# Performance work log

Measured on AMD Instinct MI355X. Metric: run time of the kernel, lower is better.

The kernel has to match this reference:

```python
import jax, jax.numpy as jnp
import numpy as np

N, H, E, T = 100000, 128, 500000, 6  # nodes, hidden, max edges, edge types


def setup_inputs() -> dict:
    key = jax.random.key(0)
    ks = jax.random.split(key, 16)
    xav_e = float(np.sqrt(6.0 / (H + T * H)))  # xavier_uniform for edge_dense
    xav_h = float(np.sqrt(6.0 / (H + H)))
    u = lambda k, s, a: jax.random.uniform(k, s, jnp.float32, -a, a)
    return {
        "node_embeddings": jax.random.normal(ks[0], (N, H), jnp.float32),
        "W_edge": u(ks[1], (H, T * H), xav_e),
        "b_edge": 1e-6 * jax.random.normal(ks[2], (T * H,), jnp.float32),
        "W_ir": u(ks[3], (H, H), xav_h), "b_ir": jnp.zeros((H,), jnp.float32),
        "W_iz": u(ks[4], (H, H), xav_h), "b_iz": jnp.zeros((H,), jnp.float32),
        "W_in": u(ks[5], (H, H), xav_h), "b_in": jnp.zeros((H,), jnp.float32),
        "W_hr": u(ks[6], (H, H), xav_h),
        "W_hz": u(ks[7], (H, H), xav_h),
        "W_hn": u(ks[8], (H, H), xav_h), "b_hn": jnp.zeros((H,), jnp.float32),
        "source_indices": jax.random.randint(ks[9], (E,), 0, N, jnp.int32),
        "dest_indices": jax.random.randint(ks[10], (E,), 0, N, jnp.int32),
        "edge_types": jax.random.randint(ks[11], (E,), 0, T, jnp.int32),
        "num_edges": 450000,
    }


def reference(node_embeddings, W_edge, b_edge, W_ir, b_ir, W_iz, b_iz,
              W_in, b_in, W_hr, W_hz, W_hn, b_hn,
              source_indices, dest_indices, edge_types, num_edges):
    num_nodes, hidden = node_embeddings.shape
    max_edges = edge_types.shape[0]
    # gather source nodes, project to all edge types at once: [E, T*H]
    src = node_embeddings[source_indices]
    all_types = (src @ W_edge + b_edge).reshape(max_edges, -1, hidden)  # [E,T,H]
    # select per-edge type
    msg = jnp.take_along_axis(all_types, edge_types[:, None, None], axis=1)[:, 0, :]
    # mask padding edges, scatter-add into destination nodes
    msg = jnp.where((jnp.arange(max_edges) < num_edges)[:, None], msg, 0)
    agg = jax.ops.segment_sum(msg, dest_indices, num_segments=num_nodes)
    # GRU update: carry h = aggregated messages, inputs x = node_embeddings
    h, x = agg, node_embeddings
    r = jax.nn.sigmoid(x @ W_ir + b_ir + h @ W_hr)
    z = jax.nn.sigmoid(x @ W_iz + b_iz + h @ W_hz)
    n = jnp.tanh(x @ W_in + b_in + r * (h @ W_hn + b_hn))
    return (1.0 - z) * n + z * h
```

## Files before the change

### kernel.cpp

```cpp
#include <hip/hip_runtime.h>
#include <hip/hip_bf16.h>

#define HD 128
#define NT 6

typedef unsigned short u16;
typedef unsigned int u32;
typedef __attribute__((ext_vector_type(8))) short bf16x8;
typedef __attribute__((ext_vector_type(4))) float f32x4;

__device__ __forceinline__ float sigmoidf_(float x) {
  return 1.0f / (1.0f + __expf(-x));
}

__device__ __forceinline__ u16 f2bf(float x) {
  u32 u = __float_as_uint(x);
  return (u16)((u + 0x7FFFu + ((u >> 16) & 1u)) >> 16);
}
__device__ __forceinline__ float bflo(u32 v) { return __uint_as_float(v << 16); }
__device__ __forceinline__ float bfhi(u32 v) { return __uint_as_float(v & 0xffff0000u); }

__device__ __forceinline__ int swz(int p) { return p ^ (((p >> 8) & 7) << 4); }

__global__ void k_cvt_w(const float* __restrict__ We,
                        const float* __restrict__ Wir, const float* __restrict__ Wiz,
                        const float* __restrict__ Win, const float* __restrict__ Whr,
                        const float* __restrict__ Whz, const float* __restrict__ Whn,
                        u16* __restrict__ WeT, u16* __restrict__ WgT) {
  int i = blockIdx.x * blockDim.x + threadIdx.x;
  if (i < NT * HD * HD) {
    int c = i >> 7, k = i & 127;
    WeT[i] = f2bf(We[(size_t)k * (NT * HD) + c]);
  } else {
    int j = i - NT * HD * HD;
    if (j < 6 * HD * HD) {
      int m = j >> 14, jj = j & 16383;
      int c = jj >> 7, k = jj & 127;
      const float* W = (m == 0) ? Wir : (m == 1) ? Wiz : (m == 2) ? Win
                     : (m == 3) ? Whr : (m == 4) ? Whz : Whn;
      WgT[j] = f2bf(W[(size_t)k * HD + c]);
    }
  }
}

__global__ __launch_bounds__(256) void k_gemm_edge6(
    const float* __restrict__ X, const u16* __restrict__ WeT,
    const float* __restrict__ Be, u16* __restrict__ P, int N)
{
  __shared__ char As[32768];
  __shared__ char Bs[32768];
  const int tid = threadIdx.x;
  const int row0 = blockIdx.x * 128;

  #pragma unroll
  for (int i = 0; i < 8; ++i) {
    int p = i * 4096 + tid * 16;
    int row = row0 + (p >> 8);
    union { u16 u[8]; bf16x8 v; } ra;
    if (row < N) {
      const float4* s = (const float4*)(X + (size_t)row0 * HD + (p >> 1));
      float4 f0 = s[0], f1 = s[1];
      ra.u[0] = f2bf(f0.x); ra.u[1] = f2bf(f0.y); ra.u[2] = f2bf(f0.z); ra.u[3] = f2bf(f0.w);
      ra.u[4] = f2bf(f1.x); ra.u[5] = f2bf(f1.y); ra.u[6] = f2bf(f1.z); ra.u[7] = f2bf(f1.w);
    } else {
      #pragma unroll
      for (int j = 0; j < 8; ++j) ra.u[j] = 0;
    }
    *(bf16x8*)(As + swz(p)) = ra.v;
  }

  const int l = tid & 63, w = tid >> 6;
  const int m0 = (w >> 1) * 64, n0 = (w & 1) * 64;
  const int lr = l & 15, lg = l >> 4;
  f32x4 zero = {0.f, 0.f, 0.f, 0.f};

  for (int t = 0; t < NT; ++t) {
    __syncthreads();
    const char* gB = (const char*)(WeT + (size_t)t * HD * HD);
    #pragma unroll
    for (int i = 0; i < 8; ++i) {
      int p = i * 4096 + tid * 16;
      *(bf16x8*)(Bs + swz(p)) = *(const bf16x8*)(gB + p);
    }
    __syncthreads();

    f32x4 acc[4][4];
    #pragma unroll
    for (int m = 0; m < 4; ++m)
      #pragma unroll
      for (int n = 0; n < 4; ++n) acc[m][n] = zero;

    #pragma unroll
    for (int k = 0; k < 4; ++k) {
      bf16x8 a[4], b[4];
      #pragma unroll
      for (int m = 0; m < 4; ++m)
        a[m] = *(const bf16x8*)(As + swz((m0 + m * 16 + lr) * 256 + k * 64 + lg * 16));
      #pragma unroll
      for (int n = 0; n < 4; ++n)
        b[n] = *(const bf16x8*)(Bs + swz((n0 + n * 16 + lr) * 256 + k * 64 + lg * 16));
      #pragma unroll
      for (int m = 0; m < 4; ++m)
        #pragma unroll
        for (int n = 0; n < 4; ++n)
          acc[m][n] = __builtin_amdgcn_mfma_f32_16x16x32_bf16(a[m], b[n], acc[m][n], 0, 0, 0);
    }

    float bias[4];
    #pragma unroll
    for (int n = 0; n < 4; ++n) bias[n] = Be[t * HD + n0 + n * 16 + lr];
    #pragma unroll
    for (int m = 0; m < 4; ++m) {
      int rbase = row0 + m0 + m * 16 + lg * 4;
      #pragma unroll
      for (int j = 0; j < 4; ++j) {
        int row = rbase + j;
        if (row < N) {
          #pragma unroll
          for (int n = 0; n < 4; ++n)
            P[(size_t)row * (NT * HD) + t * HD + n0 + n * 16 + lr] =
                f2bf(acc[m][n][j] + bias[n]);
        }
      }
    }
  }
}

__global__ __launch_bounds__(256) void k_count(const int* __restrict__ dst,
                                               const int* __restrict__ nePtr,
                                               int* __restrict__ deg) {
  const int ne = nePtr[0];
  for (int e = blockIdx.x * blockDim.x + threadIdx.x; e < ne;
       e += gridDim.x * blockDim.x)
    atomicAdd(&deg[dst[e]], 1);
}

__global__ __launch_bounds__(256) void k_scan_a(const int* __restrict__ deg,
                                                int* __restrict__ off,
                                                int* __restrict__ bsum, int N) {
  __shared__ int s[256];
  const int b = blockIdx.x, tid = threadIdx.x;
  const int base = b * 1024 + tid * 4;
  int v0 = 0, v1 = 0, v2 = 0, v3 = 0;
  if (base < N) v0 = deg[base];
  if (base + 1 < N) v1 = deg[base + 1];
  if (base + 2 < N) v2 = deg[base + 2];
  if (base + 3 < N) v3 = deg[base + 3];
  const int sum = v0 + v1 + v2 + v3;
  s[tid] = sum;
  __syncthreads();
  for (int d = 1; d < 256; d <<= 1) {
    int t = (tid >= d) ? s[tid - d] : 0;
    __syncthreads();
    s[tid] += t;
    __syncthreads();
  }
  const int excl = s[tid] - sum;
  if (base < N) off[base] = excl;
  if (base + 1 < N) off[base + 1] = excl + v0;
  if (base + 2 < N) off[base + 2] = excl + v0 + v1;
  if (base + 3 < N) off[base + 3] = excl + v0 + v1 + v2;
  if (tid == 255) bsum[b] = s[255];
}

__global__ void k_scan_b(int* __restrict__ bsum, int nb) {
  __shared__ int s[1024];
  const int tid = threadIdx.x;
  const int v = (tid < nb) ? bsum[tid] : 0;
  s[tid] = v;
  __syncthreads();
  for (int d = 1; d < 1024; d <<= 1) {
    int t = (tid >= d) ? s[tid - d] : 0;
    __syncthreads();
    s[tid] += t;
    __syncthreads();
  }
  if (tid < nb) bsum[tid] = s[tid] - v;
}

__global__ __launch_bounds__(256) void k_scan_c(int* __restrict__ off,
                                                const int* __restrict__ bsum, int N) {
  const int b = blockIdx.x, tid = threadIdx.x;
  const int add = bsum[b];
  const int base = b * 1024 + tid * 4;
  #pragma unroll
  for (int i = 0; i < 4; ++i)
    if (base + i < N) off[base + i] += add;
}

__global__ __launch_bounds__(256) void k_fill(const int* __restrict__ src,
                                              const int* __restrict__ dst,
                                              const int* __restrict__ typ,
                                              const int* __restrict__ nePtr,
                                              int* __restrict__ off,
                                              u32* __restrict__ elist) {
  const int ne = nePtr[0];
  for (int e = blockIdx.x * blockDim.x + threadIdx.x; e < ne;
       e += gridDim.x * blockDim.x) {
    int pos = atomicAdd(&off[dst[e]], 1);
    elist[pos] = (u32)(src[e] * NT + typ[e]);
  }
}

__global__ __launch_bounds__(256) void k_gather(
    const u16* __restrict__ P, const int* __restrict__ deg,
    const int* __restrict__ off, const u32* __restrict__ elist,
    u16* __restrict__ Hb, int N)
{
  const int l = threadIdx.x & 63;
  int wid = (int)((blockIdx.x * blockDim.x + threadIdx.x) >> 6);
  int nw = (int)((gridDim.x * blockDim.x) >> 6);
  for (int n = wid; n < N; n += nw) {
    const int e1 = off[n];
    const int e0 = e1 - deg[n];
    float a0 = 0.f, a1 = 0.f, b0 = 0.f, b1 = 0.f;
    for (int e = e0; e < e1; e += 4) {
      u32 p0 = elist[e];
      u32 p1 = (e + 1 < e1) ? elist[e + 1] : p0;
      u32 p2 = (e + 2 < e1) ? elist[e + 2] : p0;
      u32 p3 = (e + 3 < e1) ? elist[e + 3] : p0;
      u32 v0 = *((const u32*)(P + (size_t)p0 * HD) + l);
      u32 v1 = *((const u32*)(P + (size_t)p1 * HD) + l);
      u32 v2 = *((const u32*)(P + (size_t)p2 * HD) + l);
      u32 v3 = *((const u32*)(P + (size_t)p3 * HD) + l);
      if (e + 1 >= e1) v1 = 0;
      if (e + 2 >= e1) v2 = 0;
      if (e + 3 >= e1) v3 = 0;
      a0 += bflo(v0); a1 += bfhi(v0);
      b0 += bflo(v1); b1 += bfhi(v1);
      a0 += bflo(v2); a1 += bfhi(v2);
      b0 += bflo(v3); b1 += bfhi(v3);
    }
    a0 += b0; a1 += b1;
    u32 hp = ((u32)f2bf(a1) << 16) | (u32)f2bf(a0);
    *((u32*)(Hb + (size_t)n * HD) + l) = hp;
  }
}

__global__ __launch_bounds__(512, 2) void k_gru3(
    const float* __restrict__ X, const u16* __restrict__ Hb,
    const u16* __restrict__ WgT,
    const float* __restrict__ bir, const float* __restrict__ biz,
    const float* __restrict__ bin_, const float* __restrict__ bhn,
    float* __restrict__ out, int N)
{
  __shared__ char Xs[32768];
  __shared__ char Hs[32768];
  __shared__ char Wb[2][32768];
  const int tid = threadIdx.x;
  const int row0 = blockIdx.x * 128;
  const int l = tid & 63, w = tid >> 6;
  const int lr = l & 15, lg = l >> 4;
  const int rloc = w * 16;

  #pragma unroll
  for (int i = 0; i < 4; ++i) {
    int p = i * 8192 + tid * 16;
    int row = row0 + (p >> 8);
    union { u16 u[8]; bf16x8 v; } rx, rh;
    if (row < N) {
      const float4* sx = (const float4*)(X + (size_t)row0 * HD + (p >> 1));
      float4 x0 = sx[0], x1 = sx[1];
      rx.u[0] = f2bf(x0.x); rx.u[1] = f2bf(x0.y); rx.u[2] = f2bf(x0.z); rx.u[3] = f2bf(x0.w);
      rx.u[4] = f2bf(x1.x); rx.u[5] = f2bf(x1.y); rx.u[6] = f2bf(x1.z); rx.u[7] = f2bf(x1.w);
      rh.v = *(const bf16x8*)((const char*)Hb + (size_t)row0 * 256 + p);
    } else {
      #pragma unroll
      for (int j = 0; j < 8; ++j) { rx.u[j] = 0; rh.u[j] = 0; }
    }
    *(bf16x8*)(Xs + swz(p)) = rx.v;
    *(bf16x8*)(Hs + swz(p)) = rh.v;
  }

  bf16x8 wreg[4];
  auto loadW = [&](int g) {
    const char* gp = (const char*)(WgT + (size_t)g * HD * HD);
    #pragma unroll
    for (int i = 0; i < 4; ++i)
      wreg[i] = *(const bf16x8*)(gp + i * 8192 + tid * 16);
  };
  auto writeW = [&](int buf) {
    #pragma unroll
    for (int i = 0; i < 4; ++i) {
      int p = i * 8192 + tid * 16;
      *(bf16x8*)(Wb[buf] + swz(p)) = wreg[i];
    }
  };

  f32x4 zero = {0.f, 0.f, 0.f, 0.f};
  auto sweepL = [&](const char* Ab, const char* Wp, f32x4* acc) {
    #pragma unroll
    for (int n = 0; n < 8; ++n) acc[n] = zero;
    #pragma unroll
    for (int k = 0; k < 4; ++k) {
      bf16x8 a = *(const bf16x8*)(Ab + swz((rloc + lr) * 256 + k * 64 + lg * 16));
      #pragma unroll
      for (int n = 0; n < 8; ++n) {
        bf16x8 b = *(const bf16x8*)(Wp + swz((n * 16 + lr) * 256 + k * 64 + lg * 16));
        acc[n] = __builtin_amdgcn_mfma_f32_16x16x32_bf16(a, b, acc[n], 0, 0, 0);
      }
    }
  };

  f32x4 t1[8], t2[8], rg[8], nn[8];
  float bv[8];

  loadW(0); writeW(0);
  __syncthreads();

  loadW(3);
  sweepL(Xs, Wb[0], t1);
  writeW(1);
  __syncthreads();

  loadW(5);
  sweepL(Hs, Wb[1], t2);
  writeW(0);
  #pragma unroll
  for (int n = 0; n < 8; ++n) bv[n] = bir[n * 16 + lr];
  #pragma unroll
  for (int n = 0; n < 8; ++n)
    #pragma unroll
    for (int j = 0; j < 4; ++j) rg[n][j] = sigmoidf_(t1[n][j] + bv[n] + t2[n][j]);
  __syncthreads();

  loadW(2);
  sweepL(Hs, Wb[0], t2);
  writeW(1);
  #pragma unroll
  for (int n = 0; n < 8; ++n) bv[n] = bhn[n * 16 + lr];
  #pragma unroll
  for (int n = 0; n < 8; ++n)
    #pragma unroll
    for (int j = 0; j < 4; ++j) rg[n][j] *= (t2[n][j] + bv[n]);
  __syncthreads();

  loadW(1);
  sweepL(Xs, Wb[1], t1);
  writeW(0);
  #pragma unroll
  for (int n = 0; n < 8; ++n) bv[n] = bin_[n * 16 + lr];
  #pragma unroll
  for (int n = 0; n < 8; ++n)
    #pragma unroll
    for (int j = 0; j < 4; ++j) nn[n][j] = tanhf(t1[n][j] + bv[n] + rg[n][j]);
  __syncthreads();

  loadW(4);
  sweepL(Xs, Wb[0], t1);
  writeW(1);
  __syncthreads();

  sweepL(Hs, Wb[1], t2);
  #pragma unroll
  for (int n = 0; n < 8; ++n) bv[n] = biz[n * 16 + lr];
  #pragma unroll
  for (int n = 0; n < 8; ++n) {
    #pragma unroll
    for (int j = 0; j < 4; ++j) {
      int row = row0 + rloc + lg * 4 + j;
      if (row < N) {
        int col = n * 16 + lr;
        float z = sigmoidf_(t1[n][j] + bv[n] + t2[n][j]);
        u16 hu = Hb[(size_t)row * HD + col];
        float h = __uint_as_float((u32)hu << 16);
        out[(size_t)row * HD + col] = (1.0f - z) * nn[n][j] + z * h;
      }
    }
  }
}

__global__ __launch_bounds__(256) void k_gather_gru(
    const float* __restrict__ X, const u16* __restrict__ P,
    const int* __restrict__ deg, const int* __restrict__ off,
    const u32* __restrict__ elist, const u16* __restrict__ WgT,
    const float* __restrict__ bir, const float* __restrict__ biz,
    const float* __restrict__ bin_, const float* __restrict__ bhn,
    float* __restrict__ out, int N)
{
  __shared__ char Xs[16384];
  __shared__ char Hs[16384];
  const int tid = threadIdx.x;
  const int l = tid & 63, w = tid >> 6;
  const int row0 = blockIdx.x * 64;
  const int wr0 = w * 16;

  #pragma unroll
  for (int it = 0; it < 4; ++it) {
    int chunk = it * 64 + l;
    int r = chunk >> 4, seg = chunk & 15;
    int grow = row0 + wr0 + r;
    union { u16 u[8]; bf16x8 v; } rx;
    if (grow < N) {
      const float4* sx = (const float4*)(X + (size_t)grow * HD + seg * 8);
      float4 x0 = sx[0], x1 = sx[1];
      rx.u[0] = f2bf(x0.x); rx.u[1] = f2bf(x0.y); rx.u[2] = f2bf(x0.z); rx.u[3] = f2bf(x0.w);
      rx.u[4] = f2bf(x1.x); rx.u[5] = f2bf(x1.y); rx.u[6] = f2bf(x1.z); rx.u[7] = f2bf(x1.w);
    } else {
      #pragma unroll
      for (int j = 0; j < 8; ++j) rx.u[j] = 0;
    }
    *(bf16x8*)(Xs + swz((wr0 + r) * 256 + seg * 16)) = rx.v;
  }

  for (int i = 0; i < 16; ++i) {
    int n = row0 + wr0 + i;
    float a0 = 0.f, a1 = 0.f;
    if (n < N) {
      int e1 = off[n];
      for (int e = e1 - deg[n]; e < e1; e += 4) {
        u32 p0 = elist[e];
        u32 p1 = (e + 1 < e1) ? elist[e + 1] : p0;
        u32 p2 = (e + 2 < e1) ? elist[e + 2] : p0;
        u32 p3 = (e + 3 < e1) ? elist[e + 3] : p0;
        u32 v0 = *((const u32*)(P + (size_t)p0 * HD) + l);
        u32 v1 = *((const u32*)(P + (size_t)p1 * HD) + l);
        u32 v2 = *((const u32*)(P + (size_t)p2 * HD) + l);
        u32 v3 = *((const u32*)(P + (size_t)p3 * HD) + l);
        if (e + 1 >= e1) v1 = 0;
        if (e + 2 >= e1) v2 = 0;
        if (e + 3 >= e1) v3 = 0;
        a0 += bflo(v0) + bflo(v1) + bflo(v2) + bflo(v3);
        a1 += bfhi(v0) + bfhi(v1) + bfhi(v2) + bfhi(v3);
      }
    }
    u32 hp = ((u32)f2bf(a1) << 16) | (u32)f2bf(a0);
    *(u32*)(Hs + swz((wr0 + i) * 256 + l * 4)) = hp;
  }

  const int lr = l & 15, lg = l >> 4;
  const int rloc = wr0;

  f32x4 zero = {0.f, 0.f, 0.f, 0.f};
  auto sweep = [&](const char* Ab, const u16* WT, f32x4* acc) {
    #pragma unroll
    for (int n = 0; n < 8; ++n) acc[n] = zero;
    #pragma unroll
    for (int k = 0; k < 4; ++k) {
      bf16x8 a = *(const bf16x8*)(Ab + swz((rloc + lr) * 256 + k * 64 + lg * 16));
      #pragma unroll
      for (int n = 0; n < 8; ++n) {
        bf16x8 b = *(const bf16x8*)(WT + (size_t)(n * 16 + lr) * HD + k * 32 + lg * 8);
        acc[n] = __builtin_amdgcn_mfma_f32_16x16x32_bf16(a, b, acc[n], 0, 0, 0);
      }
    }
  };

  f32x4 t1[8], t2[8], rg[8], nn[8];
  float bv[8];

  sweep(Xs, WgT + 0 * HD * HD, t1);
  sweep(Hs, WgT + 3 * HD * HD, t2);
  #pragma unroll
  for (int n = 0; n < 8; ++n) bv[n] = bir[n * 16 + lr];
  #pragma unroll
  for (int n = 0; n < 8; ++n)
    #pragma unroll
    for (int j = 0; j < 4; ++j) rg[n][j] = sigmoidf_(t1[n][j] + bv[n] + t2[n][j]);

  sweep(Hs, WgT + 5 * HD * HD, t2);
  #pragma unroll
  for (int n = 0; n < 8; ++n) bv[n] = bhn[n * 16 + lr];
  #pragma unroll
  for (int n = 0; n < 8; ++n)
    #pragma unroll
    for (int j = 0; j < 4; ++j) rg[n][j] *= (t2[n][j] + bv[n]);

  sweep(Xs, WgT + 2 * HD * HD, t1);
  #pragma unroll
  for (int n = 0; n < 8; ++n) bv[n] = bin_[n * 16 + lr];
  #pragma unroll
  for (int n = 0; n < 8; ++n)
    #pragma unroll
    for (int j = 0; j < 4; ++j) nn[n][j] = tanhf(t1[n][j] + bv[n] + rg[n][j]);

  sweep(Xs, WgT + 1 * HD * HD, t1);
  sweep(Hs, WgT + 4 * HD * HD, t2);
  #pragma unroll
  for (int n = 0; n < 8; ++n) bv[n] = biz[n * 16 + lr];
  #pragma unroll
  for (int n = 0; n < 8; ++n) {
    #pragma unroll
    for (int j = 0; j < 4; ++j) {
      int row = row0 + rloc + lg * 4 + j;
      if (row < N) {
        float z = sigmoidf_(t1[n][j] + bv[n] + t2[n][j]);
        u16 hu = *(const u16*)(Hs + swz((rloc + lg * 4 + j) * 256 + (n * 16 + lr) * 2));
        float h = __uint_as_float((u32)hu << 16);
        out[(size_t)row * HD + n * 16 + lr] = (1.0f - z) * nn[n][j] + z * h;
      }
    }
  }
}

__global__ __launch_bounds__(256) void k_scatter(
    const u16* __restrict__ P, const int* __restrict__ src,
    const int* __restrict__ dst, const int* __restrict__ typ,
    const int* __restrict__ nePtr, float* __restrict__ agg,
    int ldP, int fixedType)
{
  const int ne = nePtr[0];
  const int lane = threadIdx.x & 63;
  const int wid = (int)((blockIdx.x * blockDim.x + threadIdx.x) >> 6);
  const int nw = (int)((gridDim.x * blockDim.x) >> 6);
  for (int e = wid; e < ne; e += nw) {
    const int t = typ[e];
    if (fixedType >= 0 && t != fixedType) continue;
    const size_t po = (ldP == HD) ? (size_t)src[e] * HD
                                  : (size_t)src[e] * (NT * HD) + (size_t)t * HD;
    u32 v = *(const u32*)(P + po + lane * 2);
    float* o = agg + (size_t)dst[e] * HD + lane * 2;
    unsafeAtomicAdd(o, bflo(v));
    unsafeAtomicAdd(o + 1, bfhi(v));
  }
}

__global__ __launch_bounds__(256) void k_gru(
    const float* __restrict__ X, const float* __restrict__ agg,
    const u16* __restrict__ WgT,
    const float* __restrict__ bir, const float* __restrict__ biz,
    const float* __restrict__ bin_, const float* __restrict__ bhn,
    float* __restrict__ out, int N)
{
  __shared__ char Xs[16384];
  __shared__ char Hs[16384];
  const int tid = threadIdx.x;
  const int row0 = blockIdx.x * 64;

  #pragma unroll
  for (int i = 0; i < 4; ++i) {
    int p = i * 4096 + tid * 16;
    int row = row0 + (p >> 8);
    union { u16 u[8]; bf16x8 v; } rx, rh;
    if (row < N) {
      const float4* sx = (const float4*)(X + (size_t)row0 * HD + (p >> 1));
      const float4* sh = (const float4*)(agg + (size_t)row0 * HD + (p >> 1));
      float4 x0 = sx[0], x1 = sx[1], h0 = sh[0], h1 = sh[1];
      rx.u[0] = f2bf(x0.x); rx.u[1] = f2bf(x0.y); rx.u[2] = f2bf(x0.z); rx.u[3] = f2bf(x0.w);
      rx.u[4] = f2bf(x1.x); rx.u[5] = f2bf(x1.y); rx.u[6] = f2bf(x1.z); rx.u[7] = f2bf(x1.w);
      rh.u[0] = f2bf(h0.x); rh.u[1] = f2bf(h0.y); rh.u[2] = f2bf(h0.z); rh.u[3] = f2bf(h0.w);
      rh.u[4] = f2bf(h1.x); rh.u[5] = f2bf(h1.y); rh.u[6] = f2bf(h1.z); rh.u[7] = f2bf(h1.w);
    } else {
      #pragma unroll
      for (int j = 0; j < 8; ++j) { rx.u[j] = 0; rh.u[j] = 0; }
    }
    *(bf16x8*)(Xs + swz(p)) = rx.v;
    *(bf16x8*)(Hs + swz(p)) = rh.v;
  }
  __syncthreads();

  const int l = tid & 63, w = tid >> 6;
  const int lr = l & 15, lg = l >> 4;
  const int rloc = w * 16;

  f32x4 zero = {0.f, 0.f, 0.f, 0.f};
  auto sweep = [&](const char* Ab, const u16* WT, f32x4* acc) {
    #pragma unroll
    for (int n = 0; n < 8; ++n) acc[n] = zero;
    #pragma unroll
    for (int k = 0; k < 4; ++k) {
      bf16x8 a = *(const bf16x8*)(Ab + swz((rloc + lr) * 256 + k * 64 + lg * 16));
      #pragma unroll
      for (int n = 0; n < 8; ++n) {
        bf16x8 b = *(const bf16x8*)(WT + (size_t)(n * 16 + lr) * HD + k * 32 + lg * 8);
        acc[n] = __builtin_amdgcn_mfma_f32_16x16x32_bf16(a, b, acc[n], 0, 0, 0);
      }
    }
  };

  f32x4 t1[8], t2[8], rg[8], nn[8];
  float bv[8];

  sweep(Xs, WgT + 0 * HD * HD, t1);
  sweep(Hs, WgT + 3 * HD * HD, t2);
  #pragma unroll
  for (int n = 0; n < 8; ++n) bv[n] = bir[n * 16 + lr];
  #pragma unroll
  for (int n = 0; n < 8; ++n)
    #pragma unroll
    for (int j = 0; j < 4; ++j) rg[n][j] = sigmoidf_(t1[n][j] + bv[n] + t2[n][j]);

  sweep(Hs, WgT + 5 * HD * HD, t2);
  #pragma unroll
  for (int n = 0; n < 8; ++n) bv[n] = bhn[n * 16 + lr];
  #pragma unroll
  for (int n = 0; n < 8; ++n)
    #pragma unroll
    for (int j = 0; j < 4; ++j) rg[n][j] *= (t2[n][j] + bv[n]);

  sweep(Xs, WgT + 2 * HD * HD, t1);
  #pragma unroll
  for (int n = 0; n < 8; ++n) bv[n] = bin_[n * 16 + lr];
  #pragma unroll
  for (int n = 0; n < 8; ++n)
    #pragma unroll
    for (int j = 0; j < 4; ++j) nn[n][j] = tanhf(t1[n][j] + bv[n] + rg[n][j]);

  sweep(Xs, WgT + 1 * HD * HD, t1);
  sweep(Hs, WgT + 4 * HD * HD, t2);
  #pragma unroll
  for (int n = 0; n < 8; ++n) bv[n] = biz[n * 16 + lr];
  #pragma unroll
  for (int n = 0; n < 8; ++n) {
    #pragma unroll
    for (int j = 0; j < 4; ++j) {
      int row = row0 + rloc + lg * 4 + j;
      if (row < N) {
        float z = sigmoidf_(t1[n][j] + bv[n] + t2[n][j]);
        float h = agg[(size_t)row * HD + n * 16 + lr];
        out[(size_t)row * HD + n * 16 + lr] = (1.0f - z) * nn[n][j] + z * h;
      }
    }
  }
}

extern "C" void kernel_launch(void* const* d_in, const int* in_sizes, int n_in,
                              void* d_out, int out_size, void* d_ws, size_t ws_size,
                              hipStream_t stream) {
  const float* X      = (const float*)d_in[0];
  const float* W_edge = (const float*)d_in[1];
  const float* b_edge = (const float*)d_in[2];
  const float* b_ir   = (const float*)d_in[4];
  const float* b_iz   = (const float*)d_in[6];
  const float* b_in   = (const float*)d_in[8];
  const float* b_hn   = (const float*)d_in[12];
  const int* src      = (const int*)d_in[13];
  const int* dst      = (const int*)d_in[14];
  const int* typ      = (const int*)d_in[15];
  const int* nePtr    = (const int*)d_in[16];

  const int N = in_sizes[0] / HD;
  const int E = in_sizes[13];
  char* ws = (char*)d_ws;

  size_t cur = 0;
  auto alloc = [&](size_t bytes) {
    size_t p = cur;
    cur = (cur + bytes + 255) & ~(size_t)255;
    return p;
  };
  u16* WeT   = (u16*)(ws + alloc((size_t)NT * HD * HD * 2));
  u16* WgT   = (u16*)(ws + alloc((size_t)6 * HD * HD * 2));
  int* deg   = (int*)(ws + alloc((size_t)N * 4));
  int* offA  = (int*)(ws + alloc((size_t)N * 4));
  int* bsum  = (int*)(ws + alloc(1024 * 4));
  u32* elist = (u32*)(ws + alloc((size_t)E * 4));
  size_t base_need = cur;
  u16* P     = (u16*)(ws + alloc((size_t)N * NT * HD * 2));
  const size_t csr_need = cur;
  u16* Hb    = (u16*)(ws + alloc((size_t)N * HD * 2));
  const size_t split_need = cur;

  const int gb = (N + 127) / 128;
  const int NB = (N + 1023) / 1024;

  k_cvt_w<<<(NT * HD * HD + 6 * HD * HD + 255) / 256, 256, 0, stream>>>(
      W_edge, (const float*)d_in[3], (const float*)d_in[5], (const float*)d_in[7],
      (const float*)d_in[9], (const float*)d_in[10], (const float*)d_in[11], WeT, WgT);

  if (ws_size >= csr_need) {
    hipMemsetAsync(deg, 0, (size_t)N * 4, stream);
    k_gemm_edge6<<<gb, 256, 0, stream>>>(X, WeT, b_edge, P, N);
    k_count<<<1024, 256, 0, stream>>>(dst, nePtr, deg);
    k_scan_a<<<NB, 256, 0, stream>>>(deg, offA, bsum, N);
    k_scan_b<<<1, 1024, 0, stream>>>(bsum, NB);
    k_scan_c<<<NB, 256, 0, stream>>>(offA, bsum, N);
    k_fill<<<1024, 256, 0, stream>>>(src, dst, typ, nePtr, offA, elist);
    if (ws_size >= split_need) {
      k_gather<<<(N + 3) / 4, 256, 0, stream>>>(P, deg, offA, elist, Hb, N);
      k_gru3<<<gb, 512, 0, stream>>>(
          X, Hb, WgT, b_ir, b_iz, b_in, b_hn, (float*)d_out, N);
    } else {
      k_gather_gru<<<(N + 63) / 64, 256, 0, stream>>>(
          X, P, deg, offA, elist, WgT, b_ir, b_iz, b_in, b_hn, (float*)d_out, N);
    }
  } else {
    float* agg = (float*)d_out;
    hipMemsetAsync(d_out, 0, (size_t)out_size * sizeof(float), stream);
    size_t pneed = base_need + (size_t)N * NT * HD * 2;
    if (ws_size >= pneed) {
      u16* Pf = (u16*)(ws + base_need);
      k_gemm_edge6<<<gb, 256, 0, stream>>>(X, WeT, b_edge, Pf, N);
      k_scatter<<<2048, 256, 0, stream>>>(Pf, src, dst, typ, nePtr, agg, NT * HD, -1);
      k_gru<<<(N + 63) / 64, 256, 0, stream>>>(X, agg, WgT, b_ir, b_iz, b_in, b_hn, agg, N);
    }
  }
}
```

Measured before the change: 253.6 us.

## Retile GRU kernel to 2x4 MFMA warp tiles with single-buffered weights

The GRU kernel now assigns each of the 8 waves a 32x64 output tile (2x4 MFMA blocks) instead of a 16x128 strip, so each wave's A and B fragment loads are reused across more MFMAs and fewer LDS reads are issued per MFMA. The double-buffered register-prefetched weight pipeline is replaced by one shared weight buffer staged with syncs before and after each load, which frees 32KB of LDS and drops the occupancy hint in launch bounds. The cost is that weight loads no longer overlap with compute, which adds sync stalls per gate matrix.

```diff
diff --git a/kernel.cpp b/kernel.cpp
--- a/kernel.cpp
+++ b/kernel.cpp
@@ -19,6 +19,7 @@
 }
 __device__ __forceinline__ float bflo(u32 v) { return __uint_as_float(v << 16); }
 __device__ __forceinline__ float bfhi(u32 v) { return __uint_as_float(v & 0xffff0000u); }
+__device__ __forceinline__ float bfs(u16 v) { return __uint_as_float((u32)v << 16); }
 
 __device__ __forceinline__ int swz(int p) { return p ^ (((p >> 8) & 7) << 4); }
 
@@ -237,7 +238,7 @@
   }
 }
 
-__global__ __launch_bounds__(512, 2) void k_gru3(
+__global__ __launch_bounds__(512) void k_gru7(
     const float* __restrict__ X, const u16* __restrict__ Hb,
     const u16* __restrict__ WgT,
     const float* __restrict__ bir, const float* __restrict__ biz,
@@ -246,12 +247,9 @@
 {
   __shared__ char Xs[32768];
   __shared__ char Hs[32768];
-  __shared__ char Wb[2][32768];
+  __shared__ char Bs[32768];
   const int tid = threadIdx.x;
   const int row0 = blockIdx.x * 128;
-  const int l = tid & 63, w = tid >> 6;
-  const int lr = l & 15, lg = l >> 4;
-  const int rloc = w * 16;
 
   #pragma unroll
   for (int i = 0; i < 4; ++i) {
@@ -272,99 +270,99 @@
     *(bf16x8*)(Hs + swz(p)) = rh.v;
   }
 
-  bf16x8 wreg[4];
-  auto loadW = [&](int g) {
-    const char* gp = (const char*)(WgT + (size_t)g * HD * HD);
-    #pragma unroll
-    for (int i = 0; i < 4; ++i)
-      wreg[i] = *(const bf16x8*)(gp + i * 8192 + tid * 16);
-  };
-  auto writeW = [&](int buf) {
+  const int l = tid & 63, w = tid >> 6;
+  const int m0 = (w >> 1) * 32;
+  const int n0 = (w & 1) * 64;
+  const int lr = l & 15, lg = l >> 4;
+  f32x4 zero = {0.f, 0.f, 0.f, 0.f};
+
+  auto stageB = [&](int g) {
+    __syncthreads();
+    const char* gB = (const char*)(WgT + (size_t)g * HD * HD);
     #pragma unroll
     for (int i = 0; i < 4; ++i) {
       int p = i * 8192 + tid * 16;
-      *(bf16x8*)(Wb[buf] + swz(p)) = wreg[i];
-    }
+      *(bf16x8*)(Bs + swz(p)) = *(const bf16x8*)(gB + p);
+    }
+    __syncthreads();
   };
 
-  f32x4 zero = {0.f, 0.f, 0.f, 0.f};
-  auto sweepL = [&](const char* Ab, const char* Wp, f32x4* acc) {
-    #pragma unroll
-    for (int n = 0; n < 8; ++n) acc[n] = zero;
+  auto sweep = [&](const char* Ab, f32x4 (&acc)[2][4]) {
+    #pragma unroll
+    for (int m = 0; m < 2; ++m)
+      #pragma unroll
+      for (int n = 0; n < 4; ++n) acc[m][n] = zero;
     #pragma unroll
     for (int k = 0; k < 4; ++k) {
-      bf16x8 a = *(const bf16x8*)(Ab + swz((rloc + lr) * 256 + k * 64 + lg * 16));
-      #pragma unroll
-      for (int n = 0; n < 8; ++n) {
-        bf16x8 b = *(const bf16x8*)(Wp + swz((n * 16 + lr) * 256 + k * 64 + lg * 16));
-        acc[n] = __builtin_amdgcn_mfma_f32_16x16x32_bf16(a, b, acc[n], 0, 0, 0);
-      }
+      bf16x8 a[2], b[4];
+      #pragma unroll
+      for (int m = 0; m < 2; ++m)
+        a[m] = *(const bf16x8*)(Ab + swz((m0 + m * 16 + lr) * 256 + k * 64 + lg * 16));
+      #pragma unroll
+      for (int n = 0; n < 4; ++n)
+        b[n] = *(const bf16x8*)(Bs + swz((n0 + n * 16 + lr) * 256 + k * 64 + lg * 16));
+      #pragma unroll
+      for (int m = 0; m < 2; ++m)
+        #pragma unroll
+        for (int n = 0; n < 4; ++n)
+          acc[m][n] = __builtin_amdgcn_mfma_f32_16x16x32_bf16(a[m], b[n], acc[m][n], 0, 0, 0);
     }
   };
 
-  f32x4 t1[8], t2[8], rg[8], nn[8];
-  float bv[8];
-
-  loadW(0); writeW(0);
-  __syncthreads();
-
-  loadW(3);
-  sweepL(Xs, Wb[0], t1);
-  writeW(1);
-  __syncthreads();
-
-  loadW(5);
-  sweepL(Hs, Wb[1], t2);
-  writeW(0);
-  #pragma unroll
-  for (int n = 0; n < 8; ++n) bv[n] = bir[n * 16 + lr];
-  #pragma unroll
-  for (int n = 0; n < 8; ++n)
-    #pragma unroll
-    for (int j = 0; j < 4; ++j) rg[n][j] = sigmoidf_(t1[n][j] + bv[n] + t2[n][j]);
-  __syncthreads();
-
-  loadW(2);
-  sweepL(Hs, Wb[0], t2);
-  writeW(1);
-  #pragma unroll
-  for (int n = 0; n < 8; ++n) bv[n] = bhn[n * 16 + lr];
-  #pragma unroll
-  for (int n = 0; n < 8; ++n)
-    #pragma unroll
-    for (int j = 0; j < 4; ++j) rg[n][j] *= (t2[n][j] + bv[n]);
-  __syncthreads();
-
-  loadW(1);
-  sweepL(Xs, Wb[1], t1);
-  writeW(0);
-  #pragma unroll
-  for (int n = 0; n < 8; ++n) bv[n] = bin_[n * 16 + lr];
-  #pragma unroll
-  for (int n = 0; n < 8; ++n)
-    #pragma unroll
-    for (int j = 0; j < 4; ++j) nn[n][j] = tanhf(t1[n][j] + bv[n] + rg[n][j]);
-  __syncthreads();
-
-  loadW(4);
-  sweepL(Xs, Wb[0], t1);
-  writeW(1);
-  __syncthreads();
-
-  sweepL(Hs, Wb[1], t2);
-  #pragma unroll
-  for (int n = 0; n < 8; ++n) bv[n] = biz[n * 16 + lr];
-  #pragma unroll
-  for (int n = 0; n < 8; ++n) {
+  f32x4 t1[2][4], t2[2][4], rg[2][4], nn[2][4];
+  float bv[4];
+  auto ldBias = [&](const float* bp) {
+    #pragma unroll
+    for (int n = 0; n < 4; ++n) bv[n] = bp[n0 + n * 16 + lr];
+  };
+
+  stageB(0); sweep(Xs, t1);
+  stageB(3); sweep(Hs, t2);
+  ldBias(bir);
+  #pragma unroll
+  for (int m = 0; m < 2; ++m)
+    #pragma unroll
+    for (int n = 0; n < 4; ++n)
+      #pragma unroll
+      for (int j = 0; j < 4; ++j)
+        rg[m][n][j] = sigmoidf_(t1[m][n][j] + bv[n] + t2[m][n][j]);
+
+  stageB(5); sweep(Hs, t2);
+  ldBias(bhn);
+  #pragma unroll
+  for (int m = 0; m < 2; ++m)
+    #pragma unroll
+    for (int n = 0; n < 4; ++n)
+      #pragma unroll
+      for (int j = 0; j < 4; ++j)
+        rg[m][n][j] *= (t2[m][n][j] + bv[n]);
+
+  stageB(2); sweep(Xs, t1);
+  ldBias(bin_);
+  #pragma unroll
+  for (int m = 0; m < 2; ++m)
+    #pragma unroll
+    for (int n = 0; n < 4; ++n)
+      #pragma unroll
+      for (int j = 0; j < 4; ++j)
+        nn[m][n][j] = tanhf(t1[m][n][j] + bv[n] + rg[m][n][j]);
+
+  stageB(1); sweep(Xs, t1);
+  stageB(4); sweep(Hs, t2);
+  ldBias(biz);
+  #pragma unroll
+  for (int m = 0; m < 2; ++m) {
     #pragma unroll
     for (int j = 0; j < 4; ++j) {
-      int row = row0 + rloc + lg * 4 + j;
+      int row = row0 + m0 + m * 16 + lg * 4 + j;
       if (row < N) {
-        int col = n * 16 + lr;
-        float z = sigmoidf_(t1[n][j] + bv[n] + t2[n][j]);
-        u16 hu = Hb[(size_t)row * HD + col];
-        float h = __uint_as_float((u32)hu << 16);
-        out[(size_t)row * HD + col] = (1.0f - z) * nn[n][j] + z * h;
+        #pragma unroll
+        for (int n = 0; n < 4; ++n) {
+          int col = n0 + n * 16 + lr;
+          float z = sigmoidf_(t1[m][n][j] + bv[n] + t2[m][n][j]);
+          float h = bfs(Hb[(size_t)row * HD + col]);
+          out[(size_t)row * HD + col] = (1.0f - z) * nn[m][n][j] + z * h;
+        }
       }
     }
   }
@@ -486,8 +484,7 @@
       if (row < N) {
         float z = sigmoidf_(t1[n][j] + bv[n] + t2[n][j]);
         u16 hu = *(const u16*)(Hs + swz((rloc + lg * 4 + j) * 256 + (n * 16 + lr) * 2));
-        float h = __uint_as_float((u32)hu << 16);
-        out[(size_t)row * HD + n * 16 + lr] = (1.0f - z) * nn[n][j] + z * h;
+        out[(size_t)row * HD + n * 16 + lr] = (1.0f - z) * nn[n][j] + z * bfs(hu);
       }
     }
   }
@@ -668,7 +665,7 @@
     k_fill<<<1024, 256, 0, stream>>>(src, dst, typ, nePtr, offA, elist);
     if (ws_size >= split_need) {
       k_gather<<<(N + 3) / 4, 256, 0, stream>>>(P, deg, offA, elist, Hb, N);
-      k_gru3<<<gb, 512, 0, stream>>>(
+      k_gru7<<<gb, 512, 0, stream>>>(
           X, Hb, WgT, b_ir, b_iz, b_in, b_hn, (float*)d_out, N);
     } else {
       k_gather_gru<<<(N + 63) / 64, 256, 0, stream>>>(
```

New measurement: 243.8 us. -3.9%, faster.
